# Kernel tuning notes

Measured on AMD Instinct MI355X. Metric: run time of the kernel, lower is better.

The kernel has to match this reference:

```python
import jax, jax.numpy as jnp
import numpy as np

IN_DIM, D, H, L = 2, 256, 8, 3
FF = 4 * D
PAST, FUT, B = 50, 20, 128
S = PAST + FUT
DH = D // H
EPS = 1e-5


def setup_inputs() -> dict:
    key = jax.random.key(0)
    ks = jax.random.split(key, 12)
    def w(k, shape, s=0.02):
        return jax.random.normal(k, shape, dtype=jnp.float32) * s
    return dict(
        past_trajectory=jax.random.normal(ks[0], (B, PAST, IN_DIM), dtype=jnp.float32),
        in_W=w(ks[1], (D, IN_DIM), 0.5), in_b=jnp.zeros((D,), jnp.float32),
        pos_emb=w(ks[2], (S, D), 1.0),
        ln0_w=jnp.ones((D,), jnp.float32), ln0_b=jnp.zeros((D,), jnp.float32),
        sa_Wqkv=w(ks[3], (L, 3 * D, D)), sa_bqkv=jnp.zeros((L, 3 * D), jnp.float32),
        sa_Wo=w(ks[4], (L, D, D)), sa_bo=jnp.zeros((L, D), jnp.float32),
        ca_Wqkv=w(ks[5], (L, 3 * D, D)), ca_bqkv=jnp.zeros((L, 3 * D), jnp.float32),
        ca_Wo=w(ks[6], (L, D, D)), ca_bo=jnp.zeros((L, D), jnp.float32),
        ff1_W=w(ks[7], (L, FF, D)), ff1_b=jnp.zeros((L, FF), jnp.float32),
        ff2_W=w(ks[8], (L, D, FF)), ff2_b=jnp.zeros((L, D), jnp.float32),
        ln1_w=jnp.ones((L, D), jnp.float32), ln1_b=jnp.zeros((L, D), jnp.float32),
        ln2_w=jnp.ones((L, D), jnp.float32), ln2_b=jnp.zeros((L, D), jnp.float32),
        ln3_w=jnp.ones((L, D), jnp.float32), ln3_b=jnp.zeros((L, D), jnp.float32),
        out_W=w(ks[9], (IN_DIM, D), 0.5), out_b=jnp.zeros((IN_DIM,), jnp.float32),
    )


def _ln(x, wt, bias):
    m = x.mean(-1, keepdims=True)
    v = ((x - m) ** 2).mean(-1, keepdims=True)  # biased var, as torch LayerNorm
    return (x - m) * jax.lax.rsqrt(v + EPS) * wt + bias


def _mha(q_in, kv_in, Wqkv, bqkv, Wo, bo, neg_mask):
    # torch nn.MultiheadAttention: packed in_proj [3D, D], y = x @ W.T + b
    Wq, Wk, Wv = Wqkv[:D], Wqkv[D:2 * D], Wqkv[2 * D:]
    bq, bk, bv = bqkv[:D], bqkv[D:2 * D], bqkv[2 * D:]
    b, s = q_in.shape[0], q_in.shape[1]
    q = (q_in @ Wq.T + bq).reshape(b, s, H, DH)
    k = (kv_in @ Wk.T + bk).reshape(b, s, H, DH)
    v = (kv_in @ Wv.T + bv).reshape(b, s, H, DH)
    scores = jnp.einsum('bqhd,bkhd->bhqk', q, k) * (1.0 / np.sqrt(DH))
    attn = jax.nn.softmax(scores + neg_mask, axis=-1)
    out = jnp.einsum('bhqk,bkhd->bqhd', attn, v).reshape(b, s, D)
    return out @ Wo.T + bo


def reference(past_trajectory, in_W, in_b, pos_emb, ln0_w, ln0_b,
              sa_Wqkv, sa_bqkv, sa_Wo, sa_bo, ca_Wqkv, ca_bqkv, ca_Wo, ca_bo,
              ff1_W, ff1_b, ff2_W, ff2_b,
              ln1_w, ln1_b, ln2_w, ln2_b, ln3_w, ln3_b, out_W, out_b):
    b = past_trajectory.shape[0]
    # deltas: zeros at t=0, then first differences
    past_deltas = jnp.concatenate(
        [jnp.zeros_like(past_trajectory[:, :1]),
         past_trajectory[:, 1:] - past_trajectory[:, :-1]], axis=1)
    causal = jnp.triu(jnp.ones((S, S), jnp.bool_), 1)
    neg_mask = jnp.where(causal, jnp.float32(-1e9), jnp.float32(0.0))[None, None]

    def full_forward(full_deltas):
        # Causal mask makes row t depend only on deltas[:, :t+1], so running at
        # the fixed padded length S reproduces the original per-step re-encode.
        x = _ln(full_deltas @ in_W.T + in_b + pos_emb[None], ln0_w, ln0_b)
        mem = x  # TransformerDecoder memory stays fixed across layers
        for l in range(L):
            x = _ln(x + _mha(x, x, sa_Wqkv[l], sa_bqkv[l], sa_Wo[l], sa_bo[l], neg_mask), ln1_w[l], ln1_b[l])
            x = _ln(x + _mha(x, mem, ca_Wqkv[l], ca_bqkv[l], ca_Wo[l], ca_bo[l], neg_mask), ln2_w[l], ln2_b[l])
            h = jax.nn.gelu(x @ ff1_W[l].T + ff1_b[l], approximate=False)
            x = _ln(x + h @ ff2_W[l].T + ff2_b[l], ln3_w[l], ln3_b[l])
        return x

    def step(carry, s_idx):
        fd, cur = carry
        out = full_forward(jnp.concatenate([past_deltas, fd], axis=1))
        row = jnp.take(out, PAST + s_idx - 1, axis=1)  # last valid position
        nd = row @ out_W.T + out_b
        fd = fd.at[:, s_idx].set(nd)
        cur = cur + nd
        return (fd, cur), cur

    init = (jnp.zeros((b, FUT, IN_DIM), past_trajectory.dtype), past_trajectory[:, -1])
    _, pos = jax.lax.scan(step, init, jnp.arange(FUT))
    return jnp.transpose(pos, (1, 0, 2))  # (B, FUT, 2)
```

## Files before the change

kernel.cpp:

```cpp
#include <hip/hip_runtime.h>
#include <hip/hip_bf16.h>

#define DMODEL 256
#define S_TOT  70
#define BATCH  128
#define HEADS  8
#define DHEAD  32
#define PAST_N 50
#define FUT_N  20
#define LAYERS 3
#define FFD    1024

#define NT 512
#define SUBT_W   192
#define TOTAL_ENT (8 * SUBT_W * 256)

__device__ __forceinline__ float wave_sum64(float v) {
#pragma unroll
  for (int off = 32; off > 0; off >>= 1) v += __shfl_xor(v, off, 64);
  return v;
}
__device__ __forceinline__ float wave_max64(float v) {
#pragma unroll
  for (int off = 32; off > 0; off >>= 1) v = fmaxf(v, __shfl_xor(v, off, 64));
  return v;
}
__device__ __forceinline__ float gelu_f(float x) {
  return 0.5f * x * (1.0f + erff(x * 0.7071067811865476f));
}
__device__ __forceinline__ uint16_t f2bf(float v) {
  uint32_t b = __float_as_uint(v);
  return (uint16_t)((b + 0x7fffu + ((b >> 16) & 1u)) >> 16);
}
__device__ __forceinline__ float bl16(uint32_t w) { return __uint_as_float(w << 16); }
__device__ __forceinline__ float bh16(uint32_t w) { return __uint_as_float(w & 0xffff0000u); }
__device__ __forceinline__ uint16_t f2h(float v) {
  _Float16 h = (_Float16)v;
  return __builtin_bit_cast(uint16_t, h);
}
__device__ __forceinline__ uint32_t pk2(float lo_, float hi_) {
  return ((uint32_t)f2h(hi_) << 16) | (uint32_t)f2h(lo_);
}
__device__ __forceinline__ float fdot2a(uint32_t a, uint32_t b, float acc) {
  asm("v_dot2_f32_f16 %0, %1, %2, %0" : "+v"(acc) : "v"(a), "v"(b));
  return acc;
}

#define SYNC() do { __builtin_amdgcn_sched_barrier(0); \
  asm volatile("s_waitcnt lgkmcnt(0)" ::: "memory"); \
  __builtin_amdgcn_s_barrier(); \
  __builtin_amdgcn_sched_barrier(0); } while (0)
#define VMWAIT8() do { __builtin_amdgcn_sched_barrier(0); \
  asm volatile("s_waitcnt vmcnt(8)" ::: "memory"); \
  __builtin_amdgcn_sched_barrier(0); } while (0)

__device__ __forceinline__ void gld_lds16(const uint4* g, uint4* l) {
  __builtin_amdgcn_global_load_lds(
      (const __attribute__((address_space(1))) void*)g,
      (__attribute__((address_space(3))) void*)l, 16, 0, 0);
}

__device__ __forceinline__ float ln_norm_256(float x, float g, float b, float* sbuf, int tid) {
  float s = wave_sum64(x);
  if ((tid & 63) == 0) sbuf[tid >> 6] = s;
  __syncthreads();
  float mean = (sbuf[0] + sbuf[1] + sbuf[2] + sbuf[3]) * (1.0f / 256.0f);
  __syncthreads();
  float d = x - mean;
  float vs = wave_sum64(d * d);
  if ((tid & 63) == 0) sbuf[tid >> 6] = vs;
  __syncthreads();
  float var = (sbuf[0] + sbuf[1] + sbuf[2] + sbuf[3]) * (1.0f / 256.0f);
  return d * rsqrtf(var + 1e-5f) * g + b;
}

#define LDK 72

__global__ __launch_bounds__(256) void k_gemm_mf(
    const float* __restrict__ A, const float* __restrict__ W,
    const float* __restrict__ bias, const float* __restrict__ Rres,
    float* __restrict__ C, int M, int N, int K, int act, int outmode,
    float* __restrict__ qout, __hip_bfloat16* __restrict__ kc,
    __hip_bfloat16* __restrict__ vc, __hip_bfloat16* __restrict__ c6,
    int rows_per_b, int pos_base)
{
  typedef __attribute__((ext_vector_type(8))) short bf8;
  typedef __attribute__((ext_vector_type(4))) float f4;
  __shared__ short Al[2][128 * LDK];
  __shared__ short Bl[2][64 * LDK];
  const int tid = threadIdx.x;
  const int wv = tid >> 6, lane = tid & 63;
  const int bm0 = blockIdx.y * 128, bn0 = blockIdx.x * 64;
  const int nkt = K >> 6;
  const int ar = tid >> 1, ah = (tid & 1) << 5;
  const int br = tid >> 2, bq = (tid & 3) << 4;

  f4 acc[2][4];
#pragma unroll
  for (int i = 0; i < 2; i++)
#pragma unroll
    for (int j = 0; j < 4; j++) acc[i][j] = (f4)0.f;

  auto stage = [&](int buf, int kt) {
    const int k0 = kt << 6;
    const float* ap = A + (size_t)(bm0 + ar) * K + k0 + ah;
    float4 av[8];
#pragma unroll
    for (int u = 0; u < 8; u++) av[u] = *(const float4*)(ap + 4 * u);
    const float* wp = W + (size_t)(bn0 + br) * K + k0 + bq;
    float4 wv4[4];
#pragma unroll
    for (int u = 0; u < 4; u++) wv4[u] = *(const float4*)(wp + 4 * u);
    short* ad = &Al[buf][ar * LDK + ah];
#pragma unroll
    for (int u = 0; u < 8; u++) {
      short4 sv = {(short)f2bf(av[u].x), (short)f2bf(av[u].y),
                   (short)f2bf(av[u].z), (short)f2bf(av[u].w)};
      *(short4*)(ad + 4 * u) = sv;
    }
    short* bd = &Bl[buf][br * LDK + bq];
#pragma unroll
    for (int u = 0; u < 4; u++) {
      short4 sv = {(short)f2bf(wv4[u].x), (short)f2bf(wv4[u].y),
                   (short)f2bf(wv4[u].z), (short)f2bf(wv4[u].w)};
      *(short4*)(bd + 4 * u) = sv;
    }
  };

  auto comp = [&](int buf) {
    const int am = wv * 32 + (lane & 15);
    const int bn = lane & 15;
    const int kb = (lane >> 4) * 8;
#pragma unroll
    for (int kk = 0; kk < 2; kk++) {
      const int ko = kk * 32 + kb;
      bf8 a0 = *(const bf8*)&Al[buf][am * LDK + ko];
      bf8 a1 = *(const bf8*)&Al[buf][(am + 16) * LDK + ko];
      bf8 b0 = *(const bf8*)&Bl[buf][bn * LDK + ko];
      bf8 b1 = *(const bf8*)&Bl[buf][(bn + 16) * LDK + ko];
      bf8 b2 = *(const bf8*)&Bl[buf][(bn + 32) * LDK + ko];
      bf8 b3 = *(const bf8*)&Bl[buf][(bn + 48) * LDK + ko];
      acc[0][0] = __builtin_amdgcn_mfma_f32_16x16x32_bf16(a0, b0, acc[0][0], 0, 0, 0);
      acc[0][1] = __builtin_amdgcn_mfma_f32_16x16x32_bf16(a0, b1, acc[0][1], 0, 0, 0);
      acc[0][2] = __builtin_amdgcn_mfma_f32_16x16x32_bf16(a0, b2, acc[0][2], 0, 0, 0);
      acc[0][3] = __builtin_amdgcn_mfma_f32_16x16x32_bf16(a0, b3, acc[0][3], 0, 0, 0);
      acc[1][0] = __builtin_amdgcn_mfma_f32_16x16x32_bf16(a1, b0, acc[1][0], 0, 0, 0);
      acc[1][1] = __builtin_amdgcn_mfma_f32_16x16x32_bf16(a1, b1, acc[1][1], 0, 0, 0);
      acc[1][2] = __builtin_amdgcn_mfma_f32_16x16x32_bf16(a1, b2, acc[1][2], 0, 0, 0);
      acc[1][3] = __builtin_amdgcn_mfma_f32_16x16x32_bf16(a1, b3, acc[1][3], 0, 0, 0);
    }
  };

  stage(0, 0);
  __syncthreads();
  for (int kt = 0; kt < nkt; kt++) {
    if (kt + 1 < nkt) stage((kt & 1) ^ 1, kt + 1);
    comp(kt & 1);
    __syncthreads();
  }

  const int n0 = bn0 + (lane & 15);
  const int r0 = bm0 + wv * 32 + (lane >> 4) * 4;
#pragma unroll
  for (int i = 0; i < 2; i++) {
#pragma unroll
    for (int r = 0; r < 4; r++) {
      const int row = r0 + i * 16 + r;
      const int b = row / rows_per_b;
      const int t = pos_base + row % rows_per_b;
#pragma unroll
      for (int j = 0; j < 4; j++) {
        const int n = n0 + j * 16;
        float v = acc[i][j][r] + bias[n];
        if (Rres) v += Rres[(size_t)row * N + n];
        if (act) v = gelu_f(v);
        if (outmode == 0) {
          C[(size_t)row * N + n] = v;
        } else if (outmode == 1) {
          if (n < 256) qout[(size_t)row * DMODEL + n] = v;
          else if (n < 512) kc[((size_t)b * S_TOT + t) * DMODEL + (n - 256)] = __float2bfloat16(v);
          else vc[((size_t)b * S_TOT + t) * DMODEL + (n - 512)] = __float2bfloat16(v);
        } else {
          const int j6 = n >> 8;
          c6[(size_t)j6 * ((size_t)BATCH * S_TOT * DMODEL) +
             ((size_t)b * S_TOT + t) * DMODEL + (n & 255)] = __float2bfloat16(v);
        }
      }
    }
  }
}

__global__ __launch_bounds__(64) void k_attn(
    const float* __restrict__ qbuf, const __hip_bfloat16* __restrict__ kc,
    const __hip_bfloat16* __restrict__ vc, float* __restrict__ outb,
    int rows_per_b, int pos_base)
{
  __shared__ float qs[DHEAD];
  __shared__ float ss[S_TOT];
  const int bid = blockIdx.x;
  const int h = bid & (HEADS - 1);
  const int row = bid >> 3;
  const int b = row / rows_per_b;
  const int t = pos_base + row % rows_per_b;
  const int nk = t + 1;
  const int lane = threadIdx.x;
  if (lane < DHEAD) qs[lane] = qbuf[(size_t)row * DMODEL + h * DHEAD + lane];
  __syncthreads();
  float mx = -1e30f;
  for (int k0 = lane; k0 < nk; k0 += 64) {
    const __hip_bfloat16* kp = kc + ((size_t)b * S_TOT + k0) * DMODEL + h * DHEAD;
    float s = 0.f;
#pragma unroll
    for (int i = 0; i < DHEAD; i++) s += qs[i] * __bfloat162float(kp[i]);
    s *= 0.17677669529663687f;
    ss[k0] = s;
    mx = fmaxf(mx, s);
  }
  mx = wave_max64(mx);
  float sum = 0.f;
  for (int k0 = lane; k0 < nk; k0 += 64) {
    float e = expf(ss[k0] - mx);
    ss[k0] = e;
    sum += e;
  }
  sum = wave_sum64(sum);
  __syncthreads();
  const float inv = 1.0f / sum;
  if (lane < DHEAD) {
    float o = 0.f;
    for (int k0 = 0; k0 < nk; k0++)
      o += ss[k0] * __bfloat162float(vc[((size_t)b * S_TOT + k0) * DMODEL + h * DHEAD + lane]);
    outb[(size_t)row * DMODEL + h * DHEAD + lane] = o * inv;
  }
}

__global__ __launch_bounds__(256) void k_ln(
    const float* __restrict__ Z, const float* __restrict__ g,
    const float* __restrict__ b, float* __restrict__ out)
{
  __shared__ float sbuf[4];
  const int row = blockIdx.x, tid = threadIdx.x;
  float x = Z[(size_t)row * DMODEL + tid];
  out[(size_t)row * DMODEL + tid] = ln_norm_256(x, g[tid], b[tid], sbuf, tid);
}

__global__ __launch_bounds__(256) void k_embed(
    const float* __restrict__ past, const float* __restrict__ in_W,
    const float* __restrict__ in_b, const float* __restrict__ pos_emb,
    const float* __restrict__ ln_w, const float* __restrict__ ln_b,
    float* __restrict__ Aout)
{
  __shared__ float sbuf[4];
  const int rowid = blockIdx.x;
  const int b = rowid / PAST_N, t = rowid % PAST_N;
  const int tid = threadIdx.x;
  float dx = 0.f, dy = 0.f;
  if (t > 0) {
    dx = past[((size_t)b * PAST_N + t) * 2 + 0] - past[((size_t)b * PAST_N + t - 1) * 2 + 0];
    dy = past[((size_t)b * PAST_N + t) * 2 + 1] - past[((size_t)b * PAST_N + t - 1) * 2 + 1];
  }
  float v = in_W[tid * 2 + 0] * dx + in_W[tid * 2 + 1] * dy + in_b[tid] +
            pos_emb[(size_t)t * DMODEL + tid];
  Aout[(size_t)rowid * DMODEL + tid] = ln_norm_256(v, ln_w[tid], ln_b[tid], sbuf, tid);
}

__global__ __launch_bounds__(256) void k_prepack(
    const float* __restrict__ caW, const float* __restrict__ cab,
    float* __restrict__ Wckv, float* __restrict__ bckv)
{
  const int n = blockIdx.x, tid = threadIdx.x;
  const int j = n >> 8, dcol = n & 255;
  const int l = j >> 1, kv = j & 1;
  const int srow = l * 768 + 256 + kv * 256 + dcol;
  Wckv[(size_t)n * 256 + tid] = caW[(size_t)srow * 256 + tid];
  if (tid == 0) bckv[n] = cab[l * 768 + 256 + kv * 256 + dcol];
}

__global__ __launch_bounds__(64) void k_readout(
    const float* __restrict__ X, const float* __restrict__ out_W,
    const float* __restrict__ out_b, const float* __restrict__ past,
    float* __restrict__ cur, float* __restrict__ ndb, float* __restrict__ out,
    int rows_per_b, int s, int init)
{
  const int b = blockIdx.x, lane = threadIdx.x;
  const int row = b * rows_per_b + rows_per_b - 1;
  float p0 = 0.f, p1 = 0.f;
  for (int d = lane; d < DMODEL; d += 64) {
    const float xv = X[(size_t)row * DMODEL + d];
    p0 += xv * out_W[d];
    p1 += xv * out_W[DMODEL + d];
  }
  p0 = wave_sum64(p0);
  p1 = wave_sum64(p1);
  if (lane == 0) {
    const float nd0 = p0 + out_b[0];
    const float nd1 = p1 + out_b[1];
    float c0, c1;
    if (init) {
      c0 = past[((size_t)b * PAST_N + PAST_N - 1) * 2 + 0];
      c1 = past[((size_t)b * PAST_N + PAST_N - 1) * 2 + 1];
    } else {
      c0 = cur[b * 2 + 0];
      c1 = cur[b * 2 + 1];
    }
    c0 += nd0; c1 += nd1;
    cur[b * 2 + 0] = c0; cur[b * 2 + 1] = c1;
    ndb[b * 2 + 0] = nd0; ndb[b * 2 + 1] = nd1;
    out[((size_t)b * FUT_N + s) * 2 + 0] = c0;
    out[((size_t)b * FUT_N + s) * 2 + 1] = c1;
  }
}

__global__ __launch_bounds__(256) void k_pack_stream(
    const float* __restrict__ sa_Wqkv, const float* __restrict__ sa_Wo,
    const float* __restrict__ ca_Wqkv, const float* __restrict__ ca_Wo,
    const float* __restrict__ ff1_W, const float* __restrict__ ff2_W,
    uint4* __restrict__ Wd)
{
  const unsigned gidx = blockIdx.x * 256 + threadIdx.x;
  if (gidx >= TOTAL_ENT) return;
  const unsigned w = gidx / (SUBT_W * 256);
  const unsigned r = gidx % (SUBT_W * 256);
  const unsigned n = r >> 8, e = r & 255u;
  const int kh = e >> 7, j = (e >> 5) & 3, c = e & 31;
  const int k8l = kh * 4 + j;
  const float* src;
  if (n < 24) {
    const int blk = n >> 2, st = n & 3;
    const int col = (int)(w * 192 + blk * 32 + c);
    const int k8 = st * 8 + k8l;
    const int j6 = col >> 8, dcol = col & 255, lq = j6 >> 1, kv = j6 & 1;
    src = ca_Wqkv + (size_t)lq * 196608 + (size_t)(256 + kv * 256 + dcol) * 256 + 8 * k8;
  } else {
    const unsigned m = n - 24;
    const int l = m / 56, p = m % 56;
    if (p < 12) {
      const int blk = p >> 2, st = p & 3;
      const int col = w * 96 + blk * 32 + c;
      const int k8 = st * 8 + k8l;
      src = sa_Wqkv + (size_t)l * 196608 + (size_t)col * 256 + 8 * k8;
    } else if (p < 16) {
      const int st = p - 12;
      const int col = w * 32 + c;
      const int k8 = st * 8 + k8l;
      src = sa_Wo + (size_t)l * 65536 + (size_t)col * 256 + 8 * k8;
    } else if (p < 20) {
      const int st = p - 16;
      const int col = w * 32 + c;
      const int k8 = st * 8 + k8l;
      src = ca_Wqkv + (size_t)l * 196608 + (size_t)col * 256 + 8 * k8;
    } else if (p < 24) {
      const int st = p - 20;
      const int col = w * 32 + c;
      const int k8 = st * 8 + k8l;
      src = ca_Wo + (size_t)l * 65536 + (size_t)col * 256 + 8 * k8;
    } else if (p < 40) {
      const int pp = p - 24;
      const int blk = pp >> 2, st = pp & 3;
      const int col = w * 128 + blk * 32 + c;
      const int k8 = st * 8 + k8l;
      src = ff1_W + (size_t)l * 262144 + (size_t)col * 256 + 8 * k8;
    } else {
      const int st = p - 40;
      const int col = w * 32 + c;
      const int k8 = st * 8 + k8l;
      src = ff2_W + (size_t)l * 262144 + (size_t)col * 1024 + 8 * k8;
    }
  }
  uint4 u;
  u.x = ((uint32_t)f2h(src[1]) << 16) | (uint32_t)f2h(src[0]);
  u.y = ((uint32_t)f2h(src[3]) << 16) | (uint32_t)f2h(src[2]);
  u.z = ((uint32_t)f2h(src[5]) << 16) | (uint32_t)f2h(src[4]);
  u.w = ((uint32_t)f2h(src[7]) << 16) | (uint32_t)f2h(src[6]);
  Wd[gidx] = u;
}

__global__ __launch_bounds__(NT) void k_decode(
    const uint4* __restrict__ Wd, const float* __restrict__ bckv,
    const float* __restrict__ in_W, const float* __restrict__ in_b,
    const float* __restrict__ pos_emb,
    const float* __restrict__ ln0_w, const float* __restrict__ ln0_b,
    const float* __restrict__ sa_bqkv, const float* __restrict__ sa_bo,
    const float* __restrict__ ca_bqkv, const float* __restrict__ ca_bo,
    const float* __restrict__ ff1_b, const float* __restrict__ ff2_b,
    const float* __restrict__ ln1_w, const float* __restrict__ ln1_b,
    const float* __restrict__ ln2_w, const float* __restrict__ ln2_b,
    const float* __restrict__ ln3_w, const float* __restrict__ ln3_b,
    const float* __restrict__ out_W, const float* __restrict__ out_b,
    __hip_bfloat16* __restrict__ Ksa, __hip_bfloat16* __restrict__ Vsa,
    __hip_bfloat16* __restrict__ C6,
    const float* __restrict__ ndb, const float* __restrict__ cur,
    float* __restrict__ out)
{
  const int b = blockIdx.x;
  const int tid = threadIdx.x;
  const int wv = tid >> 6, lane = tid & 63;
  const int sv = (wv + b) & 7;
  const size_t slab = (size_t)BATCH * S_TOT * DMODEL;

  __shared__ __align__(16) uint4 ring[8 * 4 * 256];
  __shared__ __align__(16) float x[256];
  __shared__ __align__(16) float xt[256];
  __shared__ __align__(16) float q[256];
  __shared__ __align__(16) float hbuf[1024];
  __shared__ __align__(16) float pred[256];
  __shared__ __align__(16) float kn[256], vn[256];
  __shared__ __align__(16) float ckvn[1536];
  __shared__ __align__(16) uint32_t xh[128], xth[128], atth[128], hh[512];
  __shared__ float ss[8][72];
  __shared__ float sb[8], sb2[8];
  __shared__ float ndc[4];

  const bool lo = tid < 256;
  const float c_bk0 = bckv[tid], c_bk1 = bckv[tid + 512], c_bk2 = bckv[tid + 1024];
  float c_inW0 = 0.f, c_inW1 = 0.f, c_inb = 0.f, c_l0w = 0.f, c_l0b = 0.f;
  if (lo) {
    c_inW0 = in_W[2 * tid]; c_inW1 = in_W[2 * tid + 1]; c_inb = in_b[tid];
    c_l0w = ln0_w[tid];     c_l0b = ln0_b[tid];
  }
  float bq0[LAYERS], bq1[LAYERS], bso[LAYERS], bcq[LAYERS], bco[LAYERS];
  float bf10[LAYERS], bf11[LAYERS], bf2[LAYERS];
  float w1[LAYERS], bb1[LAYERS], w2[LAYERS], bb2[LAYERS], w3[LAYERS], bb3[LAYERS];
#pragma unroll
  for (int l = 0; l < LAYERS; l++) {
    bq0[l] = sa_bqkv[l * 768 + tid];
    bq1[l] = lo ? sa_bqkv[l * 768 + 512 + tid] : 0.f;
    bso[l] = lo ? sa_bo[l * 256 + tid] : 0.f;
    bcq[l] = lo ? ca_bqkv[l * 768 + tid] : 0.f;
    bco[l] = lo ? ca_bo[l * 256 + tid] : 0.f;
    bf10[l] = ff1_b[l * 1024 + tid];
    bf11[l] = ff1_b[l * 1024 + 512 + tid];
    bf2[l] = lo ? ff2_b[l * 256 + tid] : 0.f;
    w1[l] = lo ? ln1_w[l * 256 + tid] : 0.f;  bb1[l] = lo ? ln1_b[l * 256 + tid] : 0.f;
    w2[l] = lo ? ln2_w[l * 256 + tid] : 0.f;  bb2[l] = lo ? ln2_b[l * 256 + tid] : 0.f;
    w3[l] = lo ? ln3_w[l * 256 + tid] : 0.f;  bb3[l] = lo ? ln3_b[l * 256 + tid] : 0.f;
  }
  float c_ow[4] = {0.f, 0.f, 0.f, 0.f};
  float c_ob = 0.f;
  if (tid < 128) {
    const int d0 = tid >> 6, ll = tid & 63;
#pragma unroll
    for (int j = 0; j < 4; j++) c_ow[j] = out_W[d0 * 256 + ll + 64 * j];
    c_ob = out_b[d0];
  }
  if (tid == 0) {
    ndc[0] = ndb[2 * b];     ndc[1] = ndb[2 * b + 1];
    ndc[2] = cur[2 * b];     ndc[3] = cur[2 * b + 1];
  }
  asm volatile("s_waitcnt vmcnt(0)" ::: "memory");

  auto issue = [&](unsigned g) {
    const unsigned sidx = g % (unsigned)SUBT_W;
    const unsigned slot = g & 3u;
    const uint4* src = Wd + (((size_t)sv * SUBT_W + sidx) << 8) + lane;
    uint4* dst = &ring[(((unsigned)wv << 2) | slot) * 256u + (unsigned)lane];
#pragma unroll
    for (int j = 0; j < 4; j++) gld_lds16(src + (j << 6), dst + (j << 6));
  };

  auto gemvB = [&](unsigned& g, int nblk, int nst, const uint4* xp, auto&& emit) {
    const int kh = lane >> 5, c = lane & 31;
    for (int bi = 0; bi < nblk; bi++) {
      float acc = 0.f;
      for (int st = 0; st < nst; st++) {
        VMWAIT8();
        issue(g + 3);
        const uint4* S = &ring[(((unsigned)wv << 2) | (g & 3u)) * 256u] + kh * 128 + c;
        const uint4 W0 = S[0], W1 = S[32], W2 = S[64], W3 = S[96];
        const int kb = st * 8 + kh * 4;
        const uint4 X0 = xp[kb], X1 = xp[kb + 1], X2 = xp[kb + 2], X3 = xp[kb + 3];
        acc = fdot2a(W0.x, X0.x, acc); acc = fdot2a(W0.y, X0.y, acc);
        acc = fdot2a(W0.z, X0.z, acc); acc = fdot2a(W0.w, X0.w, acc);
        acc = fdot2a(W1.x, X1.x, acc); acc = fdot2a(W1.y, X1.y, acc);
        acc = fdot2a(W1.z, X1.z, acc); acc = fdot2a(W1.w, X1.w, acc);
        acc = fdot2a(W2.x, X2.x, acc); acc = fdot2a(W2.y, X2.y, acc);
        acc = fdot2a(W2.z, X2.z, acc); acc = fdot2a(W2.w, X2.w, acc);
        acc = fdot2a(W3.x, X3.x, acc); acc = fdot2a(W3.y, X3.y, acc);
        acc = fdot2a(W3.z, X3.z, acc); acc = fdot2a(W3.w, X3.w, acc);
        g++;
      }
      acc += __shfl_xor(acc, 32, 64);
      if (lane < 32) emit(bi * 32 + c, acc);
    }
  };

  auto ln_store = [&](float v, float gw_, float gb_, float* dst, uint32_t* dsth) {
    float vv = lo ? v : 0.f;
    float s  = wave_sum64(vv);
    float s2 = wave_sum64(vv * vv);
    if ((tid & 63) == 0) { sb[tid >> 6] = s; sb2[tid >> 6] = s2; }
    SYNC();
    float mean = (sb[0] + sb[1] + sb[2] + sb[3]) * (1.0f / 256.0f);
    float ex2  = (sb2[0] + sb2[1] + sb2[2] + sb2[3]) * (1.0f / 256.0f);
    float var = ex2 - mean * mean;
    float vn_ = (vv - mean) * rsqrtf(var + 1e-5f) * gw_ + gb_;
    float vo = __shfl_xor(vn_, 1, 64);
    if (lo) {
      dst[tid] = vn_;
      if (!(tid & 1)) dsth[tid >> 1] = pk2(vn_, vo);
    }
    SYNC();
  };

  auto attn8 = [&](const __hip_bfloat16* Kc, const __hip_bfloat16* Vc,
                   const float* knw, const float* vnw, int pos) {
    const int h = wv;
    const float* qh = q + h * 32;
    float mx = -1e30f;
    for (int k0 = lane; k0 <= pos; k0 += 64) {
      float s = 0.f;
      if (k0 == pos) {
        const float* kp = knw + h * 32;
#pragma unroll
        for (int i = 0; i < 32; i++) s += qh[i] * kp[i];
      } else {
        const uint32_t* kp = (const uint32_t*)(Kc + ((size_t)b * S_TOT + k0) * DMODEL + h * 32);
#pragma unroll
        for (int i = 0; i < 16; i++) {
          uint32_t w = kp[i];
          s += bl16(w) * qh[2 * i];
          s += bh16(w) * qh[2 * i + 1];
        }
      }
      s *= 0.17677669529663687f;
      ss[h][k0] = s;
      mx = fmaxf(mx, s);
    }
    mx = wave_max64(mx);
    float sum = 0.f;
    for (int k0 = lane; k0 <= pos; k0 += 64) {
      float e = __expf(ss[h][k0] - mx);
      ss[h][k0] = e;
      sum += e;
    }
    sum = wave_sum64(sum);
    const float inv = 1.0f / sum;
    const int kpar = lane >> 4, d2 = lane & 15;
    const uint32_t* vbase = (const uint32_t*)(Vc + (size_t)b * S_TOT * DMODEL + h * 32) + d2;
    float oA = 0.f, oB = 0.f;
    for (int k0 = kpar; k0 < pos; k0 += 4) {
      const uint32_t w = vbase[(size_t)k0 * (DMODEL / 2)];
      const float p = ss[h][k0];
      oA += p * bl16(w);
      oB += p * bh16(w);
    }
    oA += __shfl_xor(oA, 16, 64); oA += __shfl_xor(oA, 32, 64);
    oB += __shfl_xor(oB, 16, 64); oB += __shfl_xor(oB, 32, 64);
    if (kpar == 0) {
      const float p = ss[h][pos];
      oA += p * vnw[h * 32 + 2 * d2];
      oB += p * vnw[h * 32 + 2 * d2 + 1];
      atth[h * 16 + d2] = pk2(oA * inv, oB * inv);
    }
  };

  unsigned g = 0;
  issue(0); issue(1); issue(2);

  for (int s = 1; s < FUT_N; s++) {
    const int pos = PAST_N - 1 + s;

    float xe = 0.f;
    if (lo) {
      xe = c_inW0 * ndc[0] + c_inW1 * ndc[1] + c_inb + pos_emb[(size_t)pos * DMODEL + tid];
    }
    ln_store(xe, c_l0w, c_l0b, xt, xth);
    if (lo) x[tid] = xt[tid];
    if (tid < 128) xh[tid] = xth[tid];

    gemvB(g, 6, 4, (const uint4*)xth, [&](int cl, float a) { ckvn[sv * 192 + cl] = a; });
    SYNC();
    {
      float v0 = ckvn[tid] + c_bk0;
      float v1 = ckvn[tid + 512] + c_bk1;
      float v2 = ckvn[tid + 1024] + c_bk2;
      ckvn[tid] = v0; ckvn[tid + 512] = v1; ckvn[tid + 1024] = v2;
      int n = tid;
      C6[(size_t)(n >> 8) * slab + ((size_t)b * S_TOT + pos) * DMODEL + (n & 255)] = __float2bfloat16(v0);
      n = tid + 512;
      C6[(size_t)(n >> 8) * slab + ((size_t)b * S_TOT + pos) * DMODEL + (n & 255)] = __float2bfloat16(v1);
      n = tid + 1024;
      C6[(size_t)(n >> 8) * slab + ((size_t)b * S_TOT + pos) * DMODEL + (n & 255)] = __float2bfloat16(v2);
      SYNC();
    }

#pragma unroll
    for (int l = 0; l < LAYERS; l++) {
      gemvB(g, 3, 4, (const uint4*)xh, [&](int cl, float a) {
        const int col = sv * 96 + cl;
        if (col < 256) q[col] = a;
        else if (col < 512) kn[col - 256] = a;
        else vn[col - 512] = a;
      });
      SYNC();
      {
        if (tid < 256) q[tid] += bq0[l];
        else {
          float v2 = kn[tid - 256] + bq0[l];
          kn[tid - 256] = v2;
          Ksa[(size_t)l * slab + ((size_t)b * S_TOT + pos) * DMODEL + (tid - 256)] = __float2bfloat16(v2);
        }
        if (lo) {
          float v2 = vn[tid] + bq1[l];
          vn[tid] = v2;
          Vsa[(size_t)l * slab + ((size_t)b * S_TOT + pos) * DMODEL + tid] = __float2bfloat16(v2);
        }
        SYNC();
      }
      attn8(Ksa + (size_t)l * slab, Vsa + (size_t)l * slab, kn, vn, pos);
      SYNC();
      gemvB(g, 1, 4, (const uint4*)atth, [&](int cl, float a) { pred[sv * 32 + cl] = a; });
      SYNC();
      ln_store(lo ? (x[tid] + pred[tid] + bso[l]) : 0.f, w1[l], bb1[l], x, xh);
      gemvB(g, 1, 4, (const uint4*)xh, [&](int cl, float a) { pred[sv * 32 + cl] = a; });
      SYNC();
      if (lo) q[tid] = pred[tid] + bcq[l];
      SYNC();
      attn8(C6 + (size_t)(2 * l) * slab, C6 + (size_t)(2 * l + 1) * slab,
            ckvn + l * 512, ckvn + l * 512 + 256, pos);
      SYNC();
      gemvB(g, 1, 4, (const uint4*)atth, [&](int cl, float a) { pred[sv * 32 + cl] = a; });
      SYNC();
      ln_store(lo ? (x[tid] + pred[tid] + bco[l]) : 0.f, w2[l], bb2[l], x, xh);
      gemvB(g, 4, 4, (const uint4*)xh, [&](int cl, float a) { hbuf[sv * 128 + cl] = a; });
      SYNC();
      {
        float g0 = gelu_f(hbuf[tid] + bf10[l]);
        float g1 = gelu_f(hbuf[tid + 512] + bf11[l]);
        float o0 = __shfl_xor(g0, 1, 64), o1 = __shfl_xor(g1, 1, 64);
        if (!(tid & 1)) {
          hh[tid >> 1] = pk2(g0, o0);
          hh[(tid + 512) >> 1] = pk2(g1, o1);
        }
        SYNC();
      }
      gemvB(g, 1, 16, (const uint4*)hh, [&](int cl, float a) { pred[sv * 32 + cl] = a; });
      SYNC();
      ln_store(lo ? (x[tid] + pred[tid] + bf2[l]) : 0.f, w3[l], bb3[l], x, xh);
    }

    {
      const int ll = tid & 63;
      if (tid < 128) {
        const int d0 = tid >> 6;
        float p = 0.f;
#pragma unroll
        for (int j = 0; j < 4; j++) p += x[ll + 64 * j] * c_ow[j];
        p = wave_sum64(p);
        if (ll == 0) {
          const float nd = p + c_ob;
          ndc[d0] = nd;
          const float c = ndc[2 + d0] + nd;
          ndc[2 + d0] = c;
          out[((size_t)b * FUT_N + s) * 2 + d0] = c;
        }
      }
      SYNC();
    }
  }
  asm volatile("s_waitcnt vmcnt(0)" ::: "memory");
}

extern "C" void kernel_launch(void* const* d_in, const int* in_sizes, int n_in,
                              void* d_out, int out_size, void* d_ws, size_t ws_size,
                              hipStream_t stream)
{
  const float* past    = (const float*)d_in[0];
  const float* in_W    = (const float*)d_in[1];
  const float* in_b    = (const float*)d_in[2];
  const float* pos_emb = (const float*)d_in[3];
  const float* ln0_w   = (const float*)d_in[4];
  const float* ln0_b   = (const float*)d_in[5];
  const float* sa_Wqkv = (const float*)d_in[6];
  const float* sa_bqkv = (const float*)d_in[7];
  const float* sa_Wo   = (const float*)d_in[8];
  const float* sa_bo   = (const float*)d_in[9];
  const float* ca_Wqkv = (const float*)d_in[10];
  const float* ca_bqkv = (const float*)d_in[11];
  const float* ca_Wo   = (const float*)d_in[12];
  const float* ca_bo   = (const float*)d_in[13];
  const float* ff1_W   = (const float*)d_in[14];
  const float* ff1_b   = (const float*)d_in[15];
  const float* ff2_W   = (const float*)d_in[16];
  const float* ff2_b   = (const float*)d_in[17];
  const float* ln1_w   = (const float*)d_in[18];
  const float* ln1_b   = (const float*)d_in[19];
  const float* ln2_w   = (const float*)d_in[20];
  const float* ln2_b   = (const float*)d_in[21];
  const float* ln3_w   = (const float*)d_in[22];
  const float* ln3_b   = (const float*)d_in[23];
  const float* out_W   = (const float*)d_in[24];
  const float* out_b   = (const float*)d_in[25];
  float* out = (float*)d_out;

  const size_t Mpre = (size_t)BATCH * PAST_N;
  const size_t slab = (size_t)BATCH * S_TOT * DMODEL;

  float* ws_f = (float*)d_ws;
  float* A    = ws_f;
  float* Bb   = A + Mpre * DMODEL;
  float* qb   = Bb + Mpre * DMODEL;
  float* at   = qb + Mpre * DMODEL;
  float* hb   = at + Mpre * DMODEL;
  float* Wckv = hb + Mpre * FFD;
  float* bckv = Wckv + (size_t)1536 * 256;
  float* ndb  = bckv + 1536;
  float* cur  = ndb + 256;
  __hip_bfloat16* Ksa = (__hip_bfloat16*)(cur + 256);
  __hip_bfloat16* Vsa = Ksa + 3 * slab;
  __hip_bfloat16* C6  = Vsa + 3 * slab;
  uint4* Wd = (uint4*)A;

  const size_t need = ((size_t)(C6 + 6 * slab) - (size_t)d_ws);
  if (ws_size < need) return;

  auto layer = [&](int l, int M, int rpb, int pbase) {
    const float* Wqkv = sa_Wqkv + (size_t)l * 768 * 256;
    __hip_bfloat16* kcl = Ksa + (size_t)l * slab;
    __hip_bfloat16* vcl = Vsa + (size_t)l * slab;
    k_gemm_mf<<<dim3(768 / 64, M / 128), 256, 0, stream>>>(
        A, Wqkv, sa_bqkv + l * 768, nullptr, nullptr, M, 768, 256, 0, 1,
        qb, kcl, vcl, nullptr, rpb, pbase);
    k_attn<<<M * HEADS, 64, 0, stream>>>(qb, kcl, vcl, at, rpb, pbase);
    k_gemm_mf<<<dim3(256 / 64, M / 128), 256, 0, stream>>>(
        at, sa_Wo + (size_t)l * 65536, sa_bo + l * 256, A, Bb, M, 256, 256, 0, 0,
        nullptr, nullptr, nullptr, nullptr, 1, 0);
    k_ln<<<M, 256, 0, stream>>>(Bb, ln1_w + l * 256, ln1_b + l * 256, A);
    k_gemm_mf<<<dim3(256 / 64, M / 128), 256, 0, stream>>>(
        A, ca_Wqkv + (size_t)l * 768 * 256, ca_bqkv + l * 768, nullptr, qb,
        M, 256, 256, 0, 0, nullptr, nullptr, nullptr, nullptr, 1, 0);
    k_attn<<<M * HEADS, 64, 0, stream>>>(
        qb, C6 + (size_t)(2 * l) * slab, C6 + (size_t)(2 * l + 1) * slab, at, rpb, pbase);
    k_gemm_mf<<<dim3(256 / 64, M / 128), 256, 0, stream>>>(
        at, ca_Wo + (size_t)l * 65536, ca_bo + l * 256, A, Bb, M, 256, 256, 0, 0,
        nullptr, nullptr, nullptr, nullptr, 1, 0);
    k_ln<<<M, 256, 0, stream>>>(Bb, ln2_w + l * 256, ln2_b + l * 256, A);
    k_gemm_mf<<<dim3(FFD / 64, M / 128), 256, 0, stream>>>(
        A, ff1_W + (size_t)l * FFD * 256, ff1_b + l * FFD, nullptr, hb,
        M, FFD, 256, 1, 0, nullptr, nullptr, nullptr, nullptr, 1, 0);
    k_gemm_mf<<<dim3(256 / 64, M / 128), 256, 0, stream>>>(
        hb, ff2_W + (size_t)l * 256 * FFD, ff2_b + l * 256, A, Bb, M, 256, FFD, 0, 0,
        nullptr, nullptr, nullptr, nullptr, 1, 0);
    k_ln<<<M, 256, 0, stream>>>(Bb, ln3_w + l * 256, ln3_b + l * 256, A);
  };

  k_prepack<<<1536, 256, 0, stream>>>(ca_Wqkv, ca_bqkv, Wckv, bckv);
  k_embed<<<(int)Mpre, 256, 0, stream>>>(past, in_W, in_b, pos_emb, ln0_w, ln0_b, A);
  k_gemm_mf<<<dim3(1536 / 64, (int)Mpre / 128), 256, 0, stream>>>(
      A, Wckv, bckv, nullptr, nullptr, (int)Mpre, 1536, 256, 0, 2,
      nullptr, nullptr, nullptr, C6, PAST_N, 0);
  for (int l = 0; l < LAYERS; l++) layer(l, (int)Mpre, PAST_N, 0);
  k_readout<<<BATCH, 64, 0, stream>>>(A, out_W, out_b, past, cur, ndb, out, PAST_N, 0, 1);

  k_pack_stream<<<(TOTAL_ENT + 255) / 256, 256, 0, stream>>>(
      sa_Wqkv, sa_Wo, ca_Wqkv, ca_Wo, ff1_W, ff2_W, Wd);

  k_decode<<<BATCH, NT, 0, stream>>>(
      Wd, bckv, in_W, in_b, pos_emb, ln0_w, ln0_b,
      sa_bqkv, sa_bo, ca_bqkv, ca_bo, ff1_b, ff2_b,
      ln1_w, ln1_b, ln2_w, ln2_b, ln3_w, ln3_b,
      out_W, out_b, Ksa, Vsa, C6, ndb, cur, out);
}
```

Measured before the change: 3.426 ms.

## Decode two batch elements per block to reuse streamed weights

The decode kernel now processes two batch rows per workgroup, launching half as many blocks. Each streamed weight tile in LDS feeds two dot-product accumulators, halving total weight traffic from global memory. The prefetch ring shrinks from 4 to 3 slots with a shallower wait depth, to keep LDS within budget now that per-row buffers are doubled. In exchange, only 64 blocks are resident, so fewer CUs are used, and the attention work per block is serialized across the two rows.

```diff
diff --git a/kernel.cpp b/kernel.cpp
--- a/kernel.cpp
+++ b/kernel.cpp
@@ -50,8 +50,8 @@
   asm volatile("s_waitcnt lgkmcnt(0)" ::: "memory"); \
   __builtin_amdgcn_s_barrier(); \
   __builtin_amdgcn_sched_barrier(0); } while (0)
-#define VMWAIT8() do { __builtin_amdgcn_sched_barrier(0); \
-  asm volatile("s_waitcnt vmcnt(8)" ::: "memory"); \
+#define VMWAIT4() do { __builtin_amdgcn_sched_barrier(0); \
+  asm volatile("s_waitcnt vmcnt(4)" ::: "memory"); \
   __builtin_amdgcn_sched_barrier(0); } while (0)
 
 __device__ __forceinline__ void gld_lds16(const uint4* g, uint4* l) {
@@ -392,120 +392,140 @@
     const float* __restrict__ ndb, const float* __restrict__ cur,
     float* __restrict__ out)
 {
-  const int b = blockIdx.x;
   const int tid = threadIdx.x;
   const int wv = tid >> 6, lane = tid & 63;
-  const int sv = (wv + b) & 7;
+  const int eb = tid >> 8, et = tid & 255;
+  const int b0 = blockIdx.x << 1;
+  const int sv = (wv + blockIdx.x) & 7;
   const size_t slab = (size_t)BATCH * S_TOT * DMODEL;
 
-  __shared__ __align__(16) uint4 ring[8 * 4 * 256];
-  __shared__ __align__(16) float x[256];
-  __shared__ __align__(16) float xt[256];
-  __shared__ __align__(16) float q[256];
-  __shared__ __align__(16) float hbuf[1024];
-  __shared__ __align__(16) float pred[256];
-  __shared__ __align__(16) float kn[256], vn[256];
-  __shared__ __align__(16) float ckvn[1536];
-  __shared__ __align__(16) uint32_t xh[128], xth[128], atth[128], hh[512];
-  __shared__ float ss[8][72];
-  __shared__ float sb[8], sb2[8];
-  __shared__ float ndc[4];
-
-  const bool lo = tid < 256;
-  const float c_bk0 = bckv[tid], c_bk1 = bckv[tid + 512], c_bk2 = bckv[tid + 1024];
-  float c_inW0 = 0.f, c_inW1 = 0.f, c_inb = 0.f, c_l0w = 0.f, c_l0b = 0.f;
-  if (lo) {
-    c_inW0 = in_W[2 * tid]; c_inW1 = in_W[2 * tid + 1]; c_inb = in_b[tid];
-    c_l0w = ln0_w[tid];     c_l0b = ln0_b[tid];
-  }
-  float bq0[LAYERS], bq1[LAYERS], bso[LAYERS], bcq[LAYERS], bco[LAYERS];
-  float bf10[LAYERS], bf11[LAYERS], bf2[LAYERS];
+  __shared__ __align__(16) uint4 ring[8 * 3 * 256];
+  __shared__ __align__(16) float x2[2][256];
+  __shared__ __align__(16) float xt2[2][256];
+  __shared__ __align__(16) float q2[2][256];
+  __shared__ __align__(16) float hbuf2[2][1024];
+  __shared__ __align__(16) float pred2[2][256];
+  __shared__ __align__(16) float kn2[2][256], vn2[2][256];
+  __shared__ __align__(16) float ckvn2[2][1536];
+  __shared__ __align__(16) uint32_t xhh[2][128], xthh[2][128], atth2[2][128], hh2[2][512];
+  __shared__ float ss2[2][8][72];
+  __shared__ float sb[8], sb2v[8];
+  __shared__ float ndc[8];
+
+  const float c_inW0 = in_W[2 * et], c_inW1 = in_W[2 * et + 1], c_inb = in_b[et];
+  const float c_l0w = ln0_w[et], c_l0b = ln0_b[et];
+  float c_bk[6];
+#pragma unroll
+  for (int d = 0; d < 6; d++) c_bk[d] = bckv[et + 256 * d];
+  float bqq[LAYERS], bqk[LAYERS], bqv[LAYERS], bso[LAYERS], bcq[LAYERS], bco[LAYERS];
+  float bf1_0[LAYERS], bf1_1[LAYERS], bf1_2[LAYERS], bf1_3[LAYERS], bf2v[LAYERS];
   float w1[LAYERS], bb1[LAYERS], w2[LAYERS], bb2[LAYERS], w3[LAYERS], bb3[LAYERS];
 #pragma unroll
   for (int l = 0; l < LAYERS; l++) {
-    bq0[l] = sa_bqkv[l * 768 + tid];
-    bq1[l] = lo ? sa_bqkv[l * 768 + 512 + tid] : 0.f;
-    bso[l] = lo ? sa_bo[l * 256 + tid] : 0.f;
-    bcq[l] = lo ? ca_bqkv[l * 768 + tid] : 0.f;
-    bco[l] = lo ? ca_bo[l * 256 + tid] : 0.f;
-    bf10[l] = ff1_b[l * 1024 + tid];
-    bf11[l] = ff1_b[l * 1024 + 512 + tid];
-    bf2[l] = lo ? ff2_b[l * 256 + tid] : 0.f;
-    w1[l] = lo ? ln1_w[l * 256 + tid] : 0.f;  bb1[l] = lo ? ln1_b[l * 256 + tid] : 0.f;
-    w2[l] = lo ? ln2_w[l * 256 + tid] : 0.f;  bb2[l] = lo ? ln2_b[l * 256 + tid] : 0.f;
-    w3[l] = lo ? ln3_w[l * 256 + tid] : 0.f;  bb3[l] = lo ? ln3_b[l * 256 + tid] : 0.f;
+    bqq[l] = sa_bqkv[l * 768 + et];
+    bqk[l] = sa_bqkv[l * 768 + 256 + et];
+    bqv[l] = sa_bqkv[l * 768 + 512 + et];
+    bso[l] = sa_bo[l * 256 + et];
+    bcq[l] = ca_bqkv[l * 768 + et];
+    bco[l] = ca_bo[l * 256 + et];
+    bf1_0[l] = ff1_b[l * 1024 + et];
+    bf1_1[l] = ff1_b[l * 1024 + 256 + et];
+    bf1_2[l] = ff1_b[l * 1024 + 512 + et];
+    bf1_3[l] = ff1_b[l * 1024 + 768 + et];
+    bf2v[l] = ff2_b[l * 256 + et];
+    w1[l] = ln1_w[l * 256 + et];  bb1[l] = ln1_b[l * 256 + et];
+    w2[l] = ln2_w[l * 256 + et];  bb2[l] = ln2_b[l * 256 + et];
+    w3[l] = ln3_w[l * 256 + et];  bb3[l] = ln3_b[l * 256 + et];
   }
   float c_ow[4] = {0.f, 0.f, 0.f, 0.f};
   float c_ob = 0.f;
-  if (tid < 128) {
-    const int d0 = tid >> 6, ll = tid & 63;
-#pragma unroll
-    for (int j = 0; j < 4; j++) c_ow[j] = out_W[d0 * 256 + ll + 64 * j];
+  if (tid < 256) {
+    const int d0 = wv & 1;
+#pragma unroll
+    for (int j = 0; j < 4; j++) c_ow[j] = out_W[d0 * 256 + lane + 64 * j];
     c_ob = out_b[d0];
   }
-  if (tid == 0) {
-    ndc[0] = ndb[2 * b];     ndc[1] = ndb[2 * b + 1];
-    ndc[2] = cur[2 * b];     ndc[3] = cur[2 * b + 1];
+  if (tid < 2) {
+    const int bb = b0 + tid;
+    ndc[tid * 4 + 0] = ndb[2 * bb];     ndc[tid * 4 + 1] = ndb[2 * bb + 1];
+    ndc[tid * 4 + 2] = cur[2 * bb];     ndc[tid * 4 + 3] = cur[2 * bb + 1];
   }
   asm volatile("s_waitcnt vmcnt(0)" ::: "memory");
+  __syncthreads();
 
   auto issue = [&](unsigned g) {
     const unsigned sidx = g % (unsigned)SUBT_W;
-    const unsigned slot = g & 3u;
+    const unsigned slot = g % 3u;
     const uint4* src = Wd + (((size_t)sv * SUBT_W + sidx) << 8) + lane;
-    uint4* dst = &ring[(((unsigned)wv << 2) | slot) * 256u + (unsigned)lane];
+    uint4* dst = &ring[((unsigned)wv * 3u + slot) * 256u + (unsigned)lane];
 #pragma unroll
     for (int j = 0; j < 4; j++) gld_lds16(src + (j << 6), dst + (j << 6));
   };
 
-  auto gemvB = [&](unsigned& g, int nblk, int nst, const uint4* xp, auto&& emit) {
+  auto gemvB = [&](unsigned& g, int nblk, int nst,
+                   const uint4* xpA, const uint4* xpB, auto&& emit) {
     const int kh = lane >> 5, c = lane & 31;
     for (int bi = 0; bi < nblk; bi++) {
-      float acc = 0.f;
+      float aA = 0.f, aB = 0.f;
       for (int st = 0; st < nst; st++) {
-        VMWAIT8();
-        issue(g + 3);
-        const uint4* S = &ring[(((unsigned)wv << 2) | (g & 3u)) * 256u] + kh * 128 + c;
+        VMWAIT4();
+        issue(g + 2);
+        const uint4* S = &ring[((unsigned)wv * 3u + (g % 3u)) * 256u] + kh * 128 + c;
         const uint4 W0 = S[0], W1 = S[32], W2 = S[64], W3 = S[96];
         const int kb = st * 8 + kh * 4;
-        const uint4 X0 = xp[kb], X1 = xp[kb + 1], X2 = xp[kb + 2], X3 = xp[kb + 3];
-        acc = fdot2a(W0.x, X0.x, acc); acc = fdot2a(W0.y, X0.y, acc);
-        acc = fdot2a(W0.z, X0.z, acc); acc = fdot2a(W0.w, X0.w, acc);
-        acc = fdot2a(W1.x, X1.x, acc); acc = fdot2a(W1.y, X1.y, acc);
-        acc = fdot2a(W1.z, X1.z, acc); acc = fdot2a(W1.w, X1.w, acc);
-        acc = fdot2a(W2.x, X2.x, acc); acc = fdot2a(W2.y, X2.y, acc);
-        acc = fdot2a(W2.z, X2.z, acc); acc = fdot2a(W2.w, X2.w, acc);
-        acc = fdot2a(W3.x, X3.x, acc); acc = fdot2a(W3.y, X3.y, acc);
-        acc = fdot2a(W3.z, X3.z, acc); acc = fdot2a(W3.w, X3.w, acc);
+        {
+          const uint4 X0 = xpA[kb], X1 = xpA[kb + 1], X2 = xpA[kb + 2], X3 = xpA[kb + 3];
+          aA = fdot2a(W0.x, X0.x, aA); aA = fdot2a(W0.y, X0.y, aA);
+          aA = fdot2a(W0.z, X0.z, aA); aA = fdot2a(W0.w, X0.w, aA);
+          aA = fdot2a(W1.x, X1.x, aA); aA = fdot2a(W1.y, X1.y, aA);
+          aA = fdot2a(W1.z, X1.z, aA); aA = fdot2a(W1.w, X1.w, aA);
+          aA = fdot2a(W2.x, X2.x, aA); aA = fdot2a(W2.y, X2.y, aA);
+          aA = fdot2a(W2.z, X2.z, aA); aA = fdot2a(W2.w, X2.w, aA);
+          aA = fdot2a(W3.x, X3.x, aA); aA = fdot2a(W3.y, X3.y, aA);
+          aA = fdot2a(W3.z, X3.z, aA); aA = fdot2a(W3.w, X3.w, aA);
+        }
+        {
+          const uint4 X0 = xpB[kb], X1 = xpB[kb + 1], X2 = xpB[kb + 2], X3 = xpB[kb + 3];
+          aB = fdot2a(W0.x, X0.x, aB); aB = fdot2a(W0.y, X0.y, aB);
+          aB = fdot2a(W0.z, X0.z, aB); aB = fdot2a(W0.w, X0.w, aB);
+          aB = fdot2a(W1.x, X1.x, aB); aB = fdot2a(W1.y, X1.y, aB);
+          aB = fdot2a(W1.z, X1.z, aB); aB = fdot2a(W1.w, X1.w, aB);
+          aB = fdot2a(W2.x, X2.x, aB); aB = fdot2a(W2.y, X2.y, aB);
+          aB = fdot2a(W2.z, X2.z, aB); aB = fdot2a(W2.w, X2.w, aB);
+          aB = fdot2a(W3.x, X3.x, aB); aB = fdot2a(W3.y, X3.y, aB);
+          aB = fdot2a(W3.z, X3.z, aB); aB = fdot2a(W3.w, X3.w, aB);
+        }
         g++;
       }
-      acc += __shfl_xor(acc, 32, 64);
-      if (lane < 32) emit(bi * 32 + c, acc);
+      aA += __shfl_xor(aA, 32, 64);
+      aB += __shfl_xor(aB, 32, 64);
+      if (lane < 32) emit(bi * 32 + c, aA, aB);
     }
   };
 
-  auto ln_store = [&](float v, float gw_, float gb_, float* dst, uint32_t* dsth) {
-    float vv = lo ? v : 0.f;
-    float s  = wave_sum64(vv);
-    float s2 = wave_sum64(vv * vv);
-    if ((tid & 63) == 0) { sb[tid >> 6] = s; sb2[tid >> 6] = s2; }
+  auto ln_store2 = [&](float v, float gw_, float gb_,
+                       float (*dstx)[256], uint32_t (*dsth)[128]) {
+    float s  = wave_sum64(v);
+    float s2 = wave_sum64(v * v);
+    if (lane == 0) { sb[wv] = s; sb2v[wv] = s2; }
     SYNC();
-    float mean = (sb[0] + sb[1] + sb[2] + sb[3]) * (1.0f / 256.0f);
-    float ex2  = (sb2[0] + sb2[1] + sb2[2] + sb2[3]) * (1.0f / 256.0f);
+    const int base = wv & 4;
+    float mean = (sb[base] + sb[base + 1] + sb[base + 2] + sb[base + 3]) * (1.0f / 256.0f);
+    float ex2  = (sb2v[base] + sb2v[base + 1] + sb2v[base + 2] + sb2v[base + 3]) * (1.0f / 256.0f);
     float var = ex2 - mean * mean;
-    float vn_ = (vv - mean) * rsqrtf(var + 1e-5f) * gw_ + gb_;
+    float vn_ = (v - mean) * rsqrtf(var + 1e-5f) * gw_ + gb_;
     float vo = __shfl_xor(vn_, 1, 64);
-    if (lo) {
-      dst[tid] = vn_;
-      if (!(tid & 1)) dsth[tid >> 1] = pk2(vn_, vo);
-    }
+    dstx[eb][et] = vn_;
+    if (!(et & 1)) dsth[eb][et >> 1] = pk2(vn_, vo);
     SYNC();
   };
 
-  auto attn8 = [&](const __hip_bfloat16* Kc, const __hip_bfloat16* Vc,
+  auto attn8 = [&](int ebb, const __hip_bfloat16* Kc, const __hip_bfloat16* Vc,
                    const float* knw, const float* vnw, int pos) {
     const int h = wv;
-    const float* qh = q + h * 32;
+    const int bb = b0 + ebb;
+    const float* qh = &q2[ebb][h * 32];
+    float* ssr = ss2[ebb][h];
     float mx = -1e30f;
     for (int k0 = lane; k0 <= pos; k0 += 64) {
       float s = 0.f;
@@ -514,7 +534,7 @@
 #pragma unroll
         for (int i = 0; i < 32; i++) s += qh[i] * kp[i];
       } else {
-        const uint32_t* kp = (const uint32_t*)(Kc + ((size_t)b * S_TOT + k0) * DMODEL + h * 32);
+        const uint32_t* kp = (const uint32_t*)(Kc + ((size_t)bb * S_TOT + k0) * DMODEL + h * 32);
 #pragma unroll
         for (int i = 0; i < 16; i++) {
           uint32_t w = kp[i];
@@ -523,136 +543,156 @@
         }
       }
       s *= 0.17677669529663687f;
-      ss[h][k0] = s;
+      ssr[k0] = s;
       mx = fmaxf(mx, s);
     }
     mx = wave_max64(mx);
     float sum = 0.f;
     for (int k0 = lane; k0 <= pos; k0 += 64) {
-      float e = __expf(ss[h][k0] - mx);
-      ss[h][k0] = e;
+      float e = __expf(ssr[k0] - mx);
+      ssr[k0] = e;
       sum += e;
     }
     sum = wave_sum64(sum);
     const float inv = 1.0f / sum;
     const int kpar = lane >> 4, d2 = lane & 15;
-    const uint32_t* vbase = (const uint32_t*)(Vc + (size_t)b * S_TOT * DMODEL + h * 32) + d2;
+    const uint32_t* vbase = (const uint32_t*)(Vc + (size_t)bb * S_TOT * DMODEL + h * 32) + d2;
     float oA = 0.f, oB = 0.f;
     for (int k0 = kpar; k0 < pos; k0 += 4) {
       const uint32_t w = vbase[(size_t)k0 * (DMODEL / 2)];
-      const float p = ss[h][k0];
+      const float p = ssr[k0];
       oA += p * bl16(w);
       oB += p * bh16(w);
     }
     oA += __shfl_xor(oA, 16, 64); oA += __shfl_xor(oA, 32, 64);
     oB += __shfl_xor(oB, 16, 64); oB += __shfl_xor(oB, 32, 64);
     if (kpar == 0) {
-      const float p = ss[h][pos];
+      const float p = ssr[pos];
       oA += p * vnw[h * 32 + 2 * d2];
       oB += p * vnw[h * 32 + 2 * d2 + 1];
-      atth[h * 16 + d2] = pk2(oA * inv, oB * inv);
+      atth2[ebb][h * 16 + d2] = pk2(oA * inv, oB * inv);
     }
   };
 
   unsigned g = 0;
-  issue(0); issue(1); issue(2);
+  issue(0); issue(1);
 
   for (int s = 1; s < FUT_N; s++) {
     const int pos = PAST_N - 1 + s;
 
-    float xe = 0.f;
-    if (lo) {
-      xe = c_inW0 * ndc[0] + c_inW1 * ndc[1] + c_inb + pos_emb[(size_t)pos * DMODEL + tid];
-    }
-    ln_store(xe, c_l0w, c_l0b, xt, xth);
-    if (lo) x[tid] = xt[tid];
-    if (tid < 128) xh[tid] = xth[tid];
-
-    gemvB(g, 6, 4, (const uint4*)xth, [&](int cl, float a) { ckvn[sv * 192 + cl] = a; });
+    float xe = c_inW0 * ndc[eb * 4 + 0] + c_inW1 * ndc[eb * 4 + 1] + c_inb +
+               pos_emb[(size_t)pos * DMODEL + et];
+    ln_store2(xe, c_l0w, c_l0b, xt2, xthh);
+    x2[eb][et] = xt2[eb][et];
+    if (et < 128) xhh[eb][et] = xthh[eb][et];
+
+    gemvB(g, 6, 4, (const uint4*)xthh[0], (const uint4*)xthh[1],
+          [&](int cl, float aA, float aB) {
+            ckvn2[0][sv * 192 + cl] = aA;
+            ckvn2[1][sv * 192 + cl] = aB;
+          });
     SYNC();
     {
-      float v0 = ckvn[tid] + c_bk0;
-      float v1 = ckvn[tid + 512] + c_bk1;
-      float v2 = ckvn[tid + 1024] + c_bk2;
-      ckvn[tid] = v0; ckvn[tid + 512] = v1; ckvn[tid + 1024] = v2;
-      int n = tid;
-      C6[(size_t)(n >> 8) * slab + ((size_t)b * S_TOT + pos) * DMODEL + (n & 255)] = __float2bfloat16(v0);
-      n = tid + 512;
-      C6[(size_t)(n >> 8) * slab + ((size_t)b * S_TOT + pos) * DMODEL + (n & 255)] = __float2bfloat16(v1);
-      n = tid + 1024;
-      C6[(size_t)(n >> 8) * slab + ((size_t)b * S_TOT + pos) * DMODEL + (n & 255)] = __float2bfloat16(v2);
+#pragma unroll
+      for (int d = 0; d < 6; d++) {
+        const int n = et + 256 * d;
+        float v = ckvn2[eb][n] + c_bk[d];
+        ckvn2[eb][n] = v;
+        C6[(size_t)d * slab + ((size_t)(b0 + eb) * S_TOT + pos) * DMODEL + et] = __float2bfloat16(v);
+      }
       SYNC();
     }
 
 #pragma unroll
     for (int l = 0; l < LAYERS; l++) {
-      gemvB(g, 3, 4, (const uint4*)xh, [&](int cl, float a) {
-        const int col = sv * 96 + cl;
-        if (col < 256) q[col] = a;
-        else if (col < 512) kn[col - 256] = a;
-        else vn[col - 512] = a;
-      });
+      gemvB(g, 3, 4, (const uint4*)xhh[0], (const uint4*)xhh[1],
+            [&](int cl, float aA, float aB) {
+              const int col = sv * 96 + cl;
+              if (col < 256) { q2[0][col] = aA; q2[1][col] = aB; }
+              else if (col < 512) { kn2[0][col - 256] = aA; kn2[1][col - 256] = aB; }
+              else { vn2[0][col - 512] = aA; vn2[1][col - 512] = aB; }
+            });
       SYNC();
       {
-        if (tid < 256) q[tid] += bq0[l];
-        else {
-          float v2 = kn[tid - 256] + bq0[l];
-          kn[tid - 256] = v2;
-          Ksa[(size_t)l * slab + ((size_t)b * S_TOT + pos) * DMODEL + (tid - 256)] = __float2bfloat16(v2);
-        }
-        if (lo) {
-          float v2 = vn[tid] + bq1[l];
-          vn[tid] = v2;
-          Vsa[(size_t)l * slab + ((size_t)b * S_TOT + pos) * DMODEL + tid] = __float2bfloat16(v2);
+        q2[eb][et] += bqq[l];
+        float kv2 = kn2[eb][et] + bqk[l];
+        kn2[eb][et] = kv2;
+        Ksa[(size_t)l * slab + ((size_t)(b0 + eb) * S_TOT + pos) * DMODEL + et] = __float2bfloat16(kv2);
+        float vv2 = vn2[eb][et] + bqv[l];
+        vn2[eb][et] = vv2;
+        Vsa[(size_t)l * slab + ((size_t)(b0 + eb) * S_TOT + pos) * DMODEL + et] = __float2bfloat16(vv2);
+        SYNC();
+      }
+      attn8(0, Ksa + (size_t)l * slab, Vsa + (size_t)l * slab, kn2[0], vn2[0], pos);
+      attn8(1, Ksa + (size_t)l * slab, Vsa + (size_t)l * slab, kn2[1], vn2[1], pos);
+      SYNC();
+      gemvB(g, 1, 4, (const uint4*)atth2[0], (const uint4*)atth2[1],
+            [&](int cl, float aA, float aB) {
+              pred2[0][sv * 32 + cl] = aA; pred2[1][sv * 32 + cl] = aB;
+            });
+      SYNC();
+      ln_store2(x2[eb][et] + pred2[eb][et] + bso[l], w1[l], bb1[l], x2, xhh);
+      gemvB(g, 1, 4, (const uint4*)xhh[0], (const uint4*)xhh[1],
+            [&](int cl, float aA, float aB) {
+              pred2[0][sv * 32 + cl] = aA; pred2[1][sv * 32 + cl] = aB;
+            });
+      SYNC();
+      q2[eb][et] = pred2[eb][et] + bcq[l];
+      SYNC();
+      attn8(0, C6 + (size_t)(2 * l) * slab, C6 + (size_t)(2 * l + 1) * slab,
+            &ckvn2[0][l * 512], &ckvn2[0][l * 512 + 256], pos);
+      attn8(1, C6 + (size_t)(2 * l) * slab, C6 + (size_t)(2 * l + 1) * slab,
+            &ckvn2[1][l * 512], &ckvn2[1][l * 512 + 256], pos);
+      SYNC();
+      gemvB(g, 1, 4, (const uint4*)atth2[0], (const uint4*)atth2[1],
+            [&](int cl, float aA, float aB) {
+              pred2[0][sv * 32 + cl] = aA; pred2[1][sv * 32 + cl] = aB;
+            });
+      SYNC();
+      ln_store2(x2[eb][et] + pred2[eb][et] + bco[l], w2[l], bb2[l], x2, xhh);
+      gemvB(g, 4, 4, (const uint4*)xhh[0], (const uint4*)xhh[1],
+            [&](int cl, float aA, float aB) {
+              hbuf2[0][sv * 128 + cl] = aA; hbuf2[1][sv * 128 + cl] = aB;
+            });
+      SYNC();
+      {
+        float g0 = gelu_f(hbuf2[eb][et] + bf1_0[l]);
+        float g1 = gelu_f(hbuf2[eb][et + 256] + bf1_1[l]);
+        float g2 = gelu_f(hbuf2[eb][et + 512] + bf1_2[l]);
+        float g3 = gelu_f(hbuf2[eb][et + 768] + bf1_3[l]);
+        float o0 = __shfl_xor(g0, 1, 64);
+        float o1 = __shfl_xor(g1, 1, 64);
+        float o2 = __shfl_xor(g2, 1, 64);
+        float o3 = __shfl_xor(g3, 1, 64);
+        if (!(et & 1)) {
+          hh2[eb][(et) >> 1]       = pk2(g0, o0);
+          hh2[eb][(et + 256) >> 1] = pk2(g1, o1);
+          hh2[eb][(et + 512) >> 1] = pk2(g2, o2);
+          hh2[eb][(et + 768) >> 1] = pk2(g3, o3);
         }
         SYNC();
       }
-      attn8(Ksa + (size_t)l * slab, Vsa + (size_t)l * slab, kn, vn, pos);
-      SYNC();
-      gemvB(g, 1, 4, (const uint4*)atth, [&](int cl, float a) { pred[sv * 32 + cl] = a; });
-      SYNC();
-      ln_store(lo ? (x[tid] + pred[tid] + bso[l]) : 0.f, w1[l], bb1[l], x, xh);
-      gemvB(g, 1, 4, (const uint4*)xh, [&](int cl, float a) { pred[sv * 32 + cl] = a; });
-      SYNC();
-      if (lo) q[tid] = pred[tid] + bcq[l];
-      SYNC();
-      attn8(C6 + (size_t)(2 * l) * slab, C6 + (size_t)(2 * l + 1) * slab,
-            ckvn + l * 512, ckvn + l * 512 + 256, pos);
-      SYNC();
-      gemvB(g, 1, 4, (const uint4*)atth, [&](int cl, float a) { pred[sv * 32 + cl] = a; });
-      SYNC();
-      ln_store(lo ? (x[tid] + pred[tid] + bco[l]) : 0.f, w2[l], bb2[l], x, xh);
-      gemvB(g, 4, 4, (const uint4*)xh, [&](int cl, float a) { hbuf[sv * 128 + cl] = a; });
-      SYNC();
-      {
-        float g0 = gelu_f(hbuf[tid] + bf10[l]);
-        float g1 = gelu_f(hbuf[tid + 512] + bf11[l]);
-        float o0 = __shfl_xor(g0, 1, 64), o1 = __shfl_xor(g1, 1, 64);
-        if (!(tid & 1)) {
-          hh[tid >> 1] = pk2(g0, o0);
-          hh[(tid + 512) >> 1] = pk2(g1, o1);
-        }
-        SYNC();
-      }
-      gemvB(g, 1, 16, (const uint4*)hh, [&](int cl, float a) { pred[sv * 32 + cl] = a; });
-      SYNC();
-      ln_store(lo ? (x[tid] + pred[tid] + bf2[l]) : 0.f, w3[l], bb3[l], x, xh);
+      gemvB(g, 1, 16, (const uint4*)hh2[0], (const uint4*)hh2[1],
+            [&](int cl, float aA, float aB) {
+              pred2[0][sv * 32 + cl] = aA; pred2[1][sv * 32 + cl] = aB;
+            });
+      SYNC();
+      ln_store2(x2[eb][et] + pred2[eb][et] + bf2v[l], w3[l], bb3[l], x2, xhh);
     }
 
     {
-      const int ll = tid & 63;
-      if (tid < 128) {
-        const int d0 = tid >> 6;
+      if (tid < 256) {
+        const int eb_r = wv >> 1, d0 = wv & 1;
         float p = 0.f;
 #pragma unroll
-        for (int j = 0; j < 4; j++) p += x[ll + 64 * j] * c_ow[j];
+        for (int j = 0; j < 4; j++) p += x2[eb_r][lane + 64 * j] * c_ow[j];
         p = wave_sum64(p);
-        if (ll == 0) {
+        if (lane == 0) {
           const float nd = p + c_ob;
-          ndc[d0] = nd;
-          const float c = ndc[2 + d0] + nd;
-          ndc[2 + d0] = c;
-          out[((size_t)b * FUT_N + s) * 2 + d0] = c;
+          ndc[eb_r * 4 + d0] = nd;
+          const float c = ndc[eb_r * 4 + 2 + d0] + nd;
+          ndc[eb_r * 4 + 2 + d0] = c;
+          out[((size_t)(b0 + eb_r) * FUT_N + s) * 2 + d0] = c;
         }
       }
       SYNC();
@@ -755,7 +795,7 @@
   k_pack_stream<<<(TOTAL_ENT + 255) / 256, 256, 0, stream>>>(
       sa_Wqkv, sa_Wo, ca_Wqkv, ca_Wo, ff1_W, ff2_W, Wd);
 
-  k_decode<<<BATCH, NT, 0, stream>>>(
+  k_decode<<<BATCH / 2, NT, 0, stream>>>(
       Wd, bckv, in_W, in_b, pos_emb, ln0_w, ln0_b,
       sa_bqkv, sa_bo, ca_bqkv, ca_bo, ff1_b, ff2_b,
       ln1_w, ln1_b, ln2_w, ln2_b, ln3_w, ln3_b,
```

Result: slower. 4.679 ms (+36.6%).
